# Optimization experiments

Hardware: AMD Instinct MI355X
Metric: run time of the kernel (lower is better)

The kernel has to match this reference:

```python
import jax, jax.numpy as jnp
import numpy as np
from jax import lax

N, E = 10000, 100000
IN_CH, HID, EDGE_DIM, K = 32, 64, 16, 3
DILATIONS = (1, 2, 4)


def setup_inputs() -> dict:
    key = jax.random.key(0)
    ks = jax.random.split(key, 20)
    def nrm(k, shape, fan):
        return jax.random.normal(k, shape, jnp.float32) * (1.0 / np.sqrt(fan))
    inp = {
        "x": jax.random.normal(ks[0], (N, IN_CH), jnp.float32),
        "edge_attr": jax.random.normal(ks[1], (E, EDGE_DIM), jnp.float32),
        "h_prev": jax.random.normal(ks[2], (N, K, HID), jnp.float32),
        "edge_index": jax.random.randint(ks[3], (2, E), 0, N, jnp.int32),
        # edge-conditioning MLP: edge_dim -> 32 -> in_ch*hid
        "w1": nrm(ks[4], (EDGE_DIM, 32), EDGE_DIM), "b1": jnp.zeros((32,), jnp.float32),
        "w2": nrm(ks[5], (32, IN_CH * HID), 32), "b2": jnp.zeros((IN_CH * HID,), jnp.float32),
        # NNConv root weight + bias
        "root": nrm(ks[6], (IN_CH, HID), IN_CH), "bias": jnp.zeros((HID,), jnp.float32),
        # three dilated Conv1d layers [out, in, k]
        "tcn_w1": nrm(ks[7], (HID, HID, K), HID * K), "tcn_b1": jnp.zeros((HID,), jnp.float32),
        "tcn_w2": nrm(ks[8], (HID, HID, K), HID * K), "tcn_b2": jnp.zeros((HID,), jnp.float32),
        "tcn_w3": nrm(ks[9], (HID, HID, K), HID * K), "tcn_b3": jnp.zeros((HID,), jnp.float32),
        # output projection hid*3 -> hid
        "proj_w": nrm(ks[10], (HID * len(DILATIONS), HID), HID * len(DILATIONS)),
        "proj_b": jnp.zeros((HID,), jnp.float32),
    }
    return inp


def _conv1d_last(h, w, b, dilation):
    # h: [N, C, L], w: [O, I, K]; 'same'-style padding (K-1)*d//2, return last timestep.
    pad = (K - 1) * dilation // 2
    out = lax.conv_general_dilated(
        h, w, window_strides=(1,), padding=[(pad, pad)],
        rhs_dilation=(dilation,), dimension_numbers=("NCH", "OIH", "NCH"))
    return out[:, :, -1] + b[None, :]


def reference(x, edge_attr, h_prev, edge_index,
              w1, b1, w2, b2, root, bias,
              tcn_w1, tcn_b1, tcn_w2, tcn_b2, tcn_w3, tcn_b3,
              proj_w, proj_b):
    src, dst = edge_index[0], edge_index[1]
    n = x.shape[0]

    # --- NNConv (ECC): per-edge weight via MLP, gather -> matmul -> scatter-mean ---
    h_e = jax.nn.relu(edge_attr @ w1 + b1)                   # [E, 32]
    W_e = (h_e @ w2 + b2).reshape(-1, IN_CH, HID)            # [E, in, hid]
    msg = jnp.einsum("ei,eio->eo", x[src], W_e)             # [E, hid]
    agg = jax.ops.segment_sum(msg, dst, num_segments=n)      # [N, hid]
    cnt = jax.ops.segment_sum(jnp.ones((msg.shape[0],), msg.dtype), dst, num_segments=n)
    mean = agg / jnp.maximum(cnt, 1.0)[:, None]
    h_graph = jax.nn.relu(mean + x @ root + bias)            # [N, hid]

    # --- history update ---
    h_hist = jnp.concatenate([h_prev[:, 1:], h_graph[:, None, :]], axis=1)  # [N, K, hid]

    # --- dilated TCN stack, keep only last timestep of each branch ---
    h_in = jnp.transpose(h_hist, (0, 2, 1))                  # [N, hid, K]
    outs = [
        _conv1d_last(h_in, tcn_w1, tcn_b1, DILATIONS[0]),
        _conv1d_last(h_in, tcn_w2, tcn_b2, DILATIONS[1]),
        _conv1d_last(h_in, tcn_w3, tcn_b3, DILATIONS[2]),
    ]
    h_cat = jnp.concatenate(outs, axis=1)                    # [N, hid*3]
    h_out = h_cat @ proj_w + proj_b                          # dropout = identity (eval)
    return h_out, h_hist
```

## Files before the change

kernel.cpp:

```cpp
#include <hip/hip_runtime.h>
#include <stdint.h>

#define NN 10000
#define NE 100000
#define CHUNK 20

__device__ __forceinline__ float bu2f(uint16_t u) {
    return __uint_as_float(((uint32_t)u) << 16);
}
__device__ __forceinline__ float blo(uint32_t v) { return __uint_as_float(v << 16); }
__device__ __forceinline__ float bhi(uint32_t v) { return __uint_as_float(v & 0xffff0000u); }
__device__ __forceinline__ uint16_t f2bu(float f) {
    uint32_t u = __float_as_uint(f);
    return (uint16_t)((u + 0x7fffu + ((u >> 16) & 1u)) >> 16);
}
__device__ __forceinline__ float ldf(const void* p, size_t i, int f32) {
    return f32 ? ((const float*)p)[i] : bu2f(((const uint16_t*)p)[i]);
}
struct f8 { float v[8]; };
__device__ __forceinline__ f8 ldf8(const void* p, size_t i, int f32) {
    f8 r;
    if (f32) {
        const float4* q = (const float4*)((const float*)p + i);
        float4 a = q[0], b = q[1];
        r.v[0]=a.x; r.v[1]=a.y; r.v[2]=a.z; r.v[3]=a.w;
        r.v[4]=b.x; r.v[5]=b.y; r.v[6]=b.z; r.v[7]=b.w;
    } else {
        uint4 u = *(const uint4*)((const uint16_t*)p + i);
        r.v[0]=blo(u.x); r.v[1]=bhi(u.x); r.v[2]=blo(u.y); r.v[3]=bhi(u.y);
        r.v[4]=blo(u.z); r.v[5]=bhi(u.z); r.v[6]=blo(u.w); r.v[7]=bhi(u.w);
    }
    return r;
}
__device__ __forceinline__ void stf(void* p, size_t i, float v, int f32) {
    if (f32) ((float*)p)[i] = v;
    else ((uint16_t*)p)[i] = f2bu(v);
}
__device__ __forceinline__ int clampi(int v, int lo, int hi) {
    return min(max(v, lo), hi);
}

__global__ __launch_bounds__(256) void k_init(
    const void* __restrict__ x, float4* __restrict__ zbase, int* __restrict__ flag)
{
    int bid = blockIdx.x;
    if (bid < 657) {
        int idx = bid * 256 + threadIdx.x;
        if (idx < 168088) zbase[idx] = make_float4(0.f, 0.f, 0.f, 0.f);
    } else if (threadIdx.x == 0) {
        const uint16_t* p = (const uint16_t*)x;
        int c = 0;
        for (int i = 0; i < 1024; i++) {
            float a = fabsf(bu2f(p[i]));
            if (a > 1e-3f && a < 16.0f) c++;
        }
        *flag = (c < 870) ? 1 : 0;
    }
}

__global__ __launch_bounds__(256) void k_prep(
    const void* __restrict__ x, const void* __restrict__ root,
    const void* __restrict__ tw1, const void* __restrict__ tw2,
    const void* __restrict__ tw3,
    const void* __restrict__ tb1, const void* __restrict__ tb2,
    const void* __restrict__ tb3,
    const void* __restrict__ proj_w,
    const void* __restrict__ edge_attr, const void* __restrict__ w1,
    const void* __restrict__ b1,
    const int* __restrict__ ei, const int* __restrict__ flag,
    float* __restrict__ xs_f, float* __restrict__ root_f,
    float* __restrict__ A, float* __restrict__ B, float* __restrict__ C,
    float* __restrict__ dv,
    int* __restrict__ outdeg, int* __restrict__ indeg,
    uint16_t* __restrict__ h_edge)
{
    int bid = blockIdx.x;
    int tid = threadIdx.x;
    if (bid < 157) {
        int f32 = *flag;
        int v8 = bid * 256 + tid;
        if (v8 < 40000) {
            f8 r = ldf8(x, (size_t)v8 * 8, f32);
            float4* o = (float4*)(xs_f + (size_t)v8 * 8);
            o[0] = make_float4(r.v[0], r.v[1], r.v[2], r.v[3]);
            o[1] = make_float4(r.v[4], r.v[5], r.v[6], r.v[7]);
        }
    } else if (bid == 157) {
        int f32 = *flag;
        f8 r = ldf8(root, (size_t)tid * 8, f32);
        float4* o = (float4*)(root_f + (size_t)tid * 8);
        o[0] = make_float4(r.v[0], r.v[1], r.v[2], r.v[3]);
        o[1] = make_float4(r.v[4], r.v[5], r.v[6], r.v[7]);
    } else if (bid < 670) {
        int f32 = *flag;
        int beta = bid - 158;
        int i = beta >> 3;
        int chunk = beta & 7;
        int o = tid & 63, sub = tid >> 6;
        int cc0 = chunk * 8 + sub * 2;
        float a = 0.f, b = 0.f, c = 0.f, d = 0.f;
        #pragma unroll
        for (int m = 0; m < 2; m++) {
            int cc = cc0 + m;
            float p0 = ldf(proj_w, (size_t)cc * 64 + o, f32);
            float p1 = ldf(proj_w, (size_t)(64 + cc) * 64 + o, f32);
            float p2 = ldf(proj_w, (size_t)(128 + cc) * 64 + o, f32);
            size_t base = (size_t)cc * 192 + i * 3;
            a = fmaf(ldf(tw1, base + 1, f32), p0, a);
            a = fmaf(ldf(tw2, base + 1, f32), p1, a);
            a = fmaf(ldf(tw3, base + 1, f32), p2, a);
            b = fmaf(ldf(tw2, base + 0, f32), p1, b);
            c = fmaf(ldf(tw1, base + 0, f32), p0, c);
            if (i == 0) {
                d = fmaf(ldf(tb1, cc, f32), p0, d);
                d = fmaf(ldf(tb2, cc, f32), p1, d);
                d = fmaf(ldf(tb3, cc, f32), p2, d);
            }
        }
        unsafeAtomicAdd(&A[i * 64 + o], a);
        unsafeAtomicAdd(&B[i * 64 + o], b);
        unsafeAtomicAdd(&C[i * 64 + o], c);
        if (i == 0) unsafeAtomicAdd(&dv[o], d);
    } else if (bid < 1061) {
        int e = (bid - 670) * 256 + tid;
        if (e < NE) {
            atomicAdd(&outdeg[clampi(ei[e], 0, NN - 1)], 1);
            atomicAdd(&indeg[clampi(ei[NE + e], 0, NN - 1)], 1);
        }
    } else {
        int f32 = *flag;
        __shared__ float w1s[512];
        __shared__ float b1s[32];
        __shared__ float eas[32][16];
        int e0 = (bid - 1061) * 32;
        if (tid < 64) {
            f8 r = ldf8(w1, (size_t)tid * 8, f32);
            #pragma unroll
            for (int q = 0; q < 8; q++) w1s[tid * 8 + q] = r.v[q];
        } else if (tid < 128) {
            int t = tid - 64;
            f8 r = ldf8(edge_attr, (size_t)e0 * 16 + (size_t)t * 8, f32);
            int el = t >> 1, half = (t & 1) * 8;
            #pragma unroll
            for (int q = 0; q < 8; q++) eas[el][half + q] = r.v[q];
        } else if (tid < 160) {
            b1s[tid - 128] = ldf(b1, tid - 128, f32);
        }
        __syncthreads();
        int el = tid >> 5, j = tid & 31;
        #pragma unroll
        for (int r = 0; r < 4; r++) {
            int e = el + r * 8;
            float acc = b1s[j];
            #pragma unroll
            for (int k = 0; k < 16; k++) acc = fmaf(eas[e][k], w1s[k * 32 + j], acc);
            h_edge[(size_t)(e0 + e) * 32 + j] = f2bu(fmaxf(acc, 0.0f));
        }
    }
}

__global__ __launch_bounds__(1024) void k_scan(
    const int* __restrict__ outdeg, int* __restrict__ offs, int* __restrict__ cursor)
{
    __shared__ int sums[1024];
    const int CH = 10;
    int tid = threadIdx.x;
    int base = tid * CH;
    int v[CH];
    int s = 0;
    #pragma unroll
    for (int k = 0; k < CH; k++) {
        int i = base + k;
        int c = (i < NN) ? outdeg[i] : 0;
        v[k] = s;
        s += c;
    }
    sums[tid] = s;
    __syncthreads();
    for (int d = 1; d < 1024; d <<= 1) {
        int t = (tid >= d) ? sums[tid - d] : 0;
        __syncthreads();
        if (tid >= d) sums[tid] += t;
        __syncthreads();
    }
    int prefix = (tid == 0) ? 0 : sums[tid - 1];
    #pragma unroll
    for (int k = 0; k < CH; k++) {
        int i = base + k;
        if (i <= NN) {
            int val = prefix + v[k];
            offs[i] = val;
            if (i < NN) cursor[i] = val;
        }
    }
}

__global__ __launch_bounds__(256, 4) void k_scatT(
    const int* __restrict__ ei, int* __restrict__ cursor,
    int* __restrict__ sorted_src, int* __restrict__ sorted_dst,
    int* __restrict__ sorted_eid,
    const uint16_t* __restrict__ h_edge, uint16_t* __restrict__ h_srt, int hs_mode,
    const float* __restrict__ xs_f, const void* __restrict__ w2,
    const void* __restrict__ b2, const int* __restrict__ flag,
    uint16_t* __restrict__ T, float* __restrict__ xb)
{
    int bid = blockIdx.x;
    int tid = threadIdx.x;
    if (bid < 391) {
        int e = bid * 256 + tid;
        if (e < NE) {
            int src = clampi(ei[e], 0, NN - 1);
            int dst = clampi(ei[NE + e], 0, NN - 1);
            int pos = clampi(atomicAdd(&cursor[src], 1), 0, NE - 1);
            sorted_src[pos] = src;
            sorted_dst[pos] = dst;
            if (hs_mode) {
                const uint4* hs = (const uint4*)(h_edge + (size_t)e * 32);
                uint4* hd = (uint4*)(h_srt + (size_t)pos * 32);
                hd[0] = hs[0]; hd[1] = hs[1]; hd[2] = hs[2]; hd[3] = hs[3];
            } else {
                sorted_eid[pos] = e;
            }
        }
        return;
    }
    int f32 = *flag;
    int n0 = (bid - 391) * 8;
    __shared__ float xs[8][32];
    xs[tid >> 5][tid & 31] = xs_f[(size_t)n0 * 32 + tid];
    __syncthreads();
    int c0 = tid * 8;
    int j = c0 >> 6, o0 = c0 & 63;
    float acc[8][8];
    #pragma unroll
    for (int s = 0; s < 8; s++)
        #pragma unroll
        for (int r = 0; r < 8; r++) acc[s][r] = 0.0f;
    if (f32) {
        const float* wb = (const float*)w2 + (size_t)j * 2048 + o0;
        for (int i = 0; i < 32; i++) {
            float4 a4 = *(const float4*)(wb + i * 64);
            float4 b4 = *(const float4*)(wb + i * 64 + 4);
            #pragma unroll
            for (int s = 0; s < 8; s++) {
                float xv = xs[s][i];
                acc[s][0] = fmaf(xv, a4.x, acc[s][0]); acc[s][1] = fmaf(xv, a4.y, acc[s][1]);
                acc[s][2] = fmaf(xv, a4.z, acc[s][2]); acc[s][3] = fmaf(xv, a4.w, acc[s][3]);
                acc[s][4] = fmaf(xv, b4.x, acc[s][4]); acc[s][5] = fmaf(xv, b4.y, acc[s][5]);
                acc[s][6] = fmaf(xv, b4.z, acc[s][6]); acc[s][7] = fmaf(xv, b4.w, acc[s][7]);
            }
        }
    } else {
        const uint16_t* wb = (const uint16_t*)w2 + (size_t)j * 2048 + o0;
        for (int i = 0; i < 32; i++) {
            uint4 u = *(const uint4*)(wb + i * 64);
            float w0 = blo(u.x), w1_ = bhi(u.x), w2_ = blo(u.y), w3 = bhi(u.y);
            float w4 = blo(u.z), w5 = bhi(u.z), w6 = blo(u.w), w7 = bhi(u.w);
            #pragma unroll
            for (int s = 0; s < 8; s++) {
                float xv = xs[s][i];
                acc[s][0] = fmaf(xv, w0, acc[s][0]); acc[s][1] = fmaf(xv, w1_, acc[s][1]);
                acc[s][2] = fmaf(xv, w2_, acc[s][2]); acc[s][3] = fmaf(xv, w3, acc[s][3]);
                acc[s][4] = fmaf(xv, w4, acc[s][4]); acc[s][5] = fmaf(xv, w5, acc[s][5]);
                acc[s][6] = fmaf(xv, w6, acc[s][6]); acc[s][7] = fmaf(xv, w7, acc[s][7]);
            }
        }
    }
    #pragma unroll
    for (int s = 0; s < 8; s++) {
        uint4 ov;
        ov.x = ((uint32_t)f2bu(acc[s][1]) << 16) | f2bu(acc[s][0]);
        ov.y = ((uint32_t)f2bu(acc[s][3]) << 16) | f2bu(acc[s][2]);
        ov.z = ((uint32_t)f2bu(acc[s][5]) << 16) | f2bu(acc[s][4]);
        ov.w = ((uint32_t)f2bu(acc[s][7]) << 16) | f2bu(acc[s][6]);
        *(uint4*)(T + (size_t)(n0 + s) * 2048 + c0) = ov;
    }
    int o = tid & 63;
    if (f32) {
        const float* b2f = (const float*)b2;
        #pragma unroll
        for (int h = 0; h < 2; h++) {
            int s = (tid >> 6) + h * 4;
            float a = 0.0f;
            #pragma unroll
            for (int i = 0; i < 32; i++)
                a = fmaf(xs[s][i], b2f[i * 64 + o], a);
            xb[(size_t)(n0 + s) * 64 + o] = a;
        }
    } else {
        const uint16_t* b2u = (const uint16_t*)b2;
        #pragma unroll
        for (int h = 0; h < 2; h++) {
            int s = (tid >> 6) + h * 4;
            float a = 0.0f;
            #pragma unroll
            for (int i = 0; i < 32; i++)
                a = fmaf(xs[s][i], bu2f(b2u[i * 64 + o]), a);
            xb[(size_t)(n0 + s) * 64 + o] = a;
        }
    }
}

__global__ __launch_bounds__(256) void k_msg_g(
    const uint16_t* __restrict__ h_edge, const uint16_t* __restrict__ h_srt,
    int hs_mode, const uint16_t* __restrict__ T,
    const float* __restrict__ xb, const int* __restrict__ sorted_src,
    const int* __restrict__ sorted_dst, const int* __restrict__ sorted_eid,
    float* __restrict__ agg)
{
    int wid = blockIdx.x * 4 + (threadIdx.x >> 6);
    int lane = threadIdx.x & 63;
    int p0 = wid * CHUNK;
    if (p0 >= NE) return;
    int p1 = min(p0 + CHUNK, NE);
    int cur = -1;
    float tv[32];
    float xbv = 0.0f;
    for (int p = p0; p < p1; p++) {
        int s = clampi(sorted_src[p], 0, NN - 1);
        if (s != cur) {
            cur = s;
            const uint16_t* Tr = T + (size_t)s * 2048 + lane;
            #pragma unroll
            for (int j = 0; j < 32; j++) tv[j] = bu2f(Tr[j * 64]);
            xbv = xb[(size_t)s * 64 + lane];
        }
        const uint4* hp;
        if (hs_mode) {
            hp = (const uint4*)(h_srt + (size_t)p * 32);
        } else {
            int e = clampi(sorted_eid[p], 0, NE - 1);
            hp = (const uint4*)(h_edge + (size_t)e * 32);
        }
        uint4 a = hp[0], b = hp[1], c = hp[2], d = hp[3];
        float s0 = 0.f, s1 = 0.f, s2 = 0.f, s3 = 0.f;
        s0 = fmaf(blo(a.x), tv[0],  s0); s0 = fmaf(bhi(a.x), tv[1],  s0);
        s0 = fmaf(blo(a.y), tv[2],  s0); s0 = fmaf(bhi(a.y), tv[3],  s0);
        s0 = fmaf(blo(a.z), tv[4],  s0); s0 = fmaf(bhi(a.z), tv[5],  s0);
        s0 = fmaf(blo(a.w), tv[6],  s0); s0 = fmaf(bhi(a.w), tv[7],  s0);
        s1 = fmaf(blo(b.x), tv[8],  s1); s1 = fmaf(bhi(b.x), tv[9],  s1);
        s1 = fmaf(blo(b.y), tv[10], s1); s1 = fmaf(bhi(b.y), tv[11], s1);
        s1 = fmaf(blo(b.z), tv[12], s1); s1 = fmaf(bhi(b.z), tv[13], s1);
        s1 = fmaf(blo(b.w), tv[14], s1); s1 = fmaf(bhi(b.w), tv[15], s1);
        s2 = fmaf(blo(c.x), tv[16], s2); s2 = fmaf(bhi(c.x), tv[17], s2);
        s2 = fmaf(blo(c.y), tv[18], s2); s2 = fmaf(bhi(c.y), tv[19], s2);
        s2 = fmaf(blo(c.z), tv[20], s2); s2 = fmaf(bhi(c.z), tv[21], s2);
        s2 = fmaf(blo(c.w), tv[22], s2); s2 = fmaf(bhi(c.w), tv[23], s2);
        s3 = fmaf(blo(d.x), tv[24], s3); s3 = fmaf(bhi(d.x), tv[25], s3);
        s3 = fmaf(blo(d.y), tv[26], s3); s3 = fmaf(bhi(d.y), tv[27], s3);
        s3 = fmaf(blo(d.z), tv[28], s3); s3 = fmaf(bhi(d.z), tv[29], s3);
        s3 = fmaf(blo(d.w), tv[30], s3); s3 = fmaf(bhi(d.w), tv[31], s3);
        float acc = xbv + (s0 + s1) + (s2 + s3);
        int dst = clampi(sorted_dst[p], 0, NN - 1);
        unsafeAtomicAdd(&agg[(size_t)dst * 64 + lane], acc);
    }
}

__global__ __launch_bounds__(256) void k_node_out(
    const float* __restrict__ agg, const int* __restrict__ indeg,
    const float* __restrict__ xs_f, const float* __restrict__ root_f,
    const void* __restrict__ bias, const void* __restrict__ h_prev,
    const float* __restrict__ A, const float* __restrict__ B,
    const float* __restrict__ C, const float* __restrict__ dv,
    const void* __restrict__ proj_b,
    const int* __restrict__ flag, void* __restrict__ out)
{
    int f32 = *flag;
    int tid = threadIdx.x;
    int s = tid >> 6, o = tid & 63;
    int n = blockIdx.x * 4 + s;
    const size_t O1 = (size_t)NN * 64;
    __shared__ float hg_s[4][64], hp1_s[4][64], hp2_s[4][64];

    float xr = 0.0f;
    const float* xp = xs_f + (size_t)n * 32;
    #pragma unroll
    for (int i = 0; i < 32; i++)
        xr = fmaf(xp[i], root_f[i * 64 + o], xr);
    float c = (float)indeg[n];
    float m = agg[(size_t)n * 64 + o] / fmaxf(c, 1.0f);
    float hg = fmaxf(m + xr + ldf(bias, o, f32), 0.0f);
    float hp1 = ldf(h_prev, (size_t)n * 192 + 64 + o, f32);
    float hp2 = ldf(h_prev, (size_t)n * 192 + 128 + o, f32);
    hg_s[s][o] = hg; hp1_s[s][o] = hp1; hp2_s[s][o] = hp2;
    stf(out, O1 + (size_t)n * 192 + o, hp1, f32);
    stf(out, O1 + (size_t)n * 192 + 64 + o, hp2, f32);
    stf(out, O1 + (size_t)n * 192 + 128 + o, hg, f32);
    __syncthreads();

    float accA = 0.f, accB = 0.f, accC = 0.f;
    #pragma unroll 8
    for (int i = 0; i < 64; i++) {
        accA = fmaf(hg_s[s][i],  A[i * 64 + o], accA);
        accB = fmaf(hp1_s[s][i], B[i * 64 + o], accB);
        accC = fmaf(hp2_s[s][i], C[i * 64 + o], accC);
    }
    float acc = dv[o] + ldf(proj_b, o, f32) + (accA + accB) + accC;
    stf(out, (size_t)n * 64 + o, acc, f32);
}

static inline size_t align64(size_t v) { return (v + 63) & ~(size_t)63; }

extern "C" void kernel_launch(void* const* d_in, const int* in_sizes, int n_in,
                              void* d_out, int out_size, void* d_ws, size_t ws_size,
                              hipStream_t stream) {
    const void* x         = d_in[0];
    const void* edge_attr = d_in[1];
    const void* h_prev    = d_in[2];
    const int*  ei        = (const int*)d_in[3];
    const void* w1     = d_in[4];
    const void* b1     = d_in[5];
    const void* w2     = d_in[6];
    const void* b2     = d_in[7];
    const void* root   = d_in[8];
    const void* bias   = d_in[9];
    const void* tw1    = d_in[10];
    const void* tb1    = d_in[11];
    const void* tw2    = d_in[12];
    const void* tb2    = d_in[13];
    const void* tw3    = d_in[14];
    const void* tb3    = d_in[15];
    const void* proj_w = d_in[16];
    const void* proj_b = d_in[17];

    char* ws = (char*)d_ws;
    size_t off = 0;
    uint16_t* T      = (uint16_t*)(ws + off); off = align64(off + (size_t)NN * 2048 * 2);
    uint16_t* h_edge = (uint16_t*)(ws + off); off = align64(off + (size_t)NE * 32 * 2);
    float* xs_f   = (float*)(ws + off); off = align64(off + (size_t)NN * 32 * 4);
    float* root_f = (float*)(ws + off); off = align64(off + (size_t)2048 * 4);
    float* xb     = (float*)(ws + off); off = align64(off + (size_t)NN * 64 * 4);
    size_t zero_base = off;
    float* agg    = (float*)(ws + off); off = align64(off + (size_t)NN * 64 * 4);
    int* indeg    = (int*)(ws + off);   off = align64(off + (size_t)NN * 4);
    int* outdeg   = (int*)(ws + off);   off = align64(off + (size_t)NN * 4);
    float* Amat   = (float*)(ws + off); off = align64(off + (size_t)4096 * 4);
    float* Bmat   = (float*)(ws + off); off = align64(off + (size_t)4096 * 4);
    float* Cmat   = (float*)(ws + off); off = align64(off + (size_t)4096 * 4);
    float* dvec   = (float*)(ws + off); off = align64(off + (size_t)64 * 4);
    int* offs        = (int*)(ws + off); off = align64(off + (size_t)(NN + 1) * 4);
    int* cursor      = (int*)(ws + off); off = align64(off + (size_t)NN * 4);
    int* sorted_src  = (int*)(ws + off); off = align64(off + (size_t)NE * 4);
    int* sorted_dst  = (int*)(ws + off); off = align64(off + (size_t)NE * 4);
    int* sorted_eid  = (int*)(ws + off); off = align64(off + (size_t)NE * 4);
    int* flag        = (int*)(ws + off); off = align64(off + 64);
    uint16_t* h_srt  = (uint16_t*)(ws + off);
    size_t off_end = off + (size_t)NE * 32 * 2;
    int hs_mode = (off_end <= ws_size) ? 1 : 0;

    k_init<<<658, 256, 0, stream>>>(x, (float4*)((char*)d_ws + zero_base), flag);
    k_prep<<<4186, 256, 0, stream>>>(x, root, tw1, tw2, tw3, tb1, tb2, tb3,
                                     proj_w, edge_attr, w1, b1, ei, flag,
                                     xs_f, root_f, Amat, Bmat, Cmat, dvec,
                                     outdeg, indeg, h_edge);
    k_scan<<<1, 1024, 0, stream>>>(outdeg, offs, cursor);
    k_scatT<<<391 + NN / 8, 256, 0, stream>>>(ei, cursor, sorted_src, sorted_dst,
                                              sorted_eid, h_edge, h_srt, hs_mode,
                                              xs_f, w2, b2, flag, T, xb);
    k_msg_g<<<(NE / CHUNK + 3) / 4, 256, 0, stream>>>(h_edge, h_srt, hs_mode, T, xb,
                                                      sorted_src, sorted_dst,
                                                      sorted_eid, agg);
    k_node_out<<<NN / 4, 256, 0, stream>>>(agg, indeg, xs_f, root_f, bias, h_prev,
                                           Amat, Bmat, Cmat, dvec, proj_b, flag, d_out);
}
```

Baseline: 225.9 us.

## Move per-node T/xb precompute into prep kernel and prefetch edges in message loop

Moves the per-node x·W2 (T) and x·b2 (xb) computation out of the scatter kernel into extra blocks of the prep kernel, reading x directly, so it overlaps with other prep work and the scatter kernel becomes a lightweight sort. The message kernel now software-prefetches the next edge's hidden vector and source index, and halves CHUNK to give more parallel blocks. The edge MLP caches w1 columns in registers, and the prep kernel gains a launch-bounds occupancy hint. The trade-offs are more atomic contention on agg from smaller chunks and higher register pressure in prep.

```diff
diff --git a/kernel.cpp b/kernel.cpp
--- a/kernel.cpp
+++ b/kernel.cpp
@@ -3,7 +3,7 @@
 
 #define NN 10000
 #define NE 100000
-#define CHUNK 20
+#define CHUNK 10
 
 __device__ __forceinline__ float bu2f(uint16_t u) {
     return __uint_as_float(((uint32_t)u) << 16);
@@ -58,7 +58,7 @@
     }
 }
 
-__global__ __launch_bounds__(256) void k_prep(
+__global__ __launch_bounds__(256, 4) void k_prep(
     const void* __restrict__ x, const void* __restrict__ root,
     const void* __restrict__ tw1, const void* __restrict__ tw2,
     const void* __restrict__ tw3,
@@ -67,12 +67,14 @@
     const void* __restrict__ proj_w,
     const void* __restrict__ edge_attr, const void* __restrict__ w1,
     const void* __restrict__ b1,
+    const void* __restrict__ w2, const void* __restrict__ b2,
     const int* __restrict__ ei, const int* __restrict__ flag,
     float* __restrict__ xs_f, float* __restrict__ root_f,
     float* __restrict__ A, float* __restrict__ B, float* __restrict__ C,
     float* __restrict__ dv,
     int* __restrict__ outdeg, int* __restrict__ indeg,
-    uint16_t* __restrict__ h_edge)
+    uint16_t* __restrict__ h_edge,
+    uint16_t* __restrict__ T, float* __restrict__ xb)
 {
     int bid = blockIdx.x;
     int tid = threadIdx.x;
@@ -127,7 +129,7 @@
             atomicAdd(&outdeg[clampi(ei[e], 0, NN - 1)], 1);
             atomicAdd(&indeg[clampi(ei[NE + e], 0, NN - 1)], 1);
         }
-    } else {
+    } else if (bid < 4186) {
         int f32 = *flag;
         __shared__ float w1s[512];
         __shared__ float b1s[32];
@@ -148,13 +150,98 @@
         }
         __syncthreads();
         int el = tid >> 5, j = tid & 31;
+        float wreg[16];
+        #pragma unroll
+        for (int k = 0; k < 16; k++) wreg[k] = w1s[k * 32 + j];
+        float bj = b1s[j];
         #pragma unroll
         for (int r = 0; r < 4; r++) {
             int e = el + r * 8;
-            float acc = b1s[j];
-            #pragma unroll
-            for (int k = 0; k < 16; k++) acc = fmaf(eas[e][k], w1s[k * 32 + j], acc);
+            float acc = bj;
+            #pragma unroll
+            for (int k = 0; k < 16; k++) acc = fmaf(eas[e][k], wreg[k], acc);
             h_edge[(size_t)(e0 + e) * 32 + j] = f2bu(fmaxf(acc, 0.0f));
+        }
+    } else {
+        int f32 = *flag;
+        int n0 = (bid - 4186) * 8;
+        __shared__ float xs[8][32];
+        if (tid < 32) {
+            f8 r = ldf8(x, (size_t)n0 * 32 + (size_t)tid * 8, f32);
+            int base = tid * 8;
+            #pragma unroll
+            for (int q = 0; q < 8; q++) xs[(base + q) >> 5][(base + q) & 31] = r.v[q];
+        }
+        __syncthreads();
+        int c0 = tid * 8;
+        int j = c0 >> 6, o0 = c0 & 63;
+        float acc[8][8];
+        #pragma unroll
+        for (int s = 0; s < 8; s++)
+            #pragma unroll
+            for (int r = 0; r < 8; r++) acc[s][r] = 0.0f;
+        if (f32) {
+            const float* wb = (const float*)w2 + (size_t)j * 2048 + o0;
+            for (int i = 0; i < 32; i++) {
+                float4 a4 = *(const float4*)(wb + i * 64);
+                float4 b4 = *(const float4*)(wb + i * 64 + 4);
+                #pragma unroll
+                for (int s = 0; s < 8; s++) {
+                    float xv = xs[s][i];
+                    acc[s][0] = fmaf(xv, a4.x, acc[s][0]); acc[s][1] = fmaf(xv, a4.y, acc[s][1]);
+                    acc[s][2] = fmaf(xv, a4.z, acc[s][2]); acc[s][3] = fmaf(xv, a4.w, acc[s][3]);
+                    acc[s][4] = fmaf(xv, b4.x, acc[s][4]); acc[s][5] = fmaf(xv, b4.y, acc[s][5]);
+                    acc[s][6] = fmaf(xv, b4.z, acc[s][6]); acc[s][7] = fmaf(xv, b4.w, acc[s][7]);
+                }
+            }
+        } else {
+            const uint16_t* wb = (const uint16_t*)w2 + (size_t)j * 2048 + o0;
+            for (int i = 0; i < 32; i++) {
+                uint4 u = *(const uint4*)(wb + i * 64);
+                float w0 = blo(u.x), w1_ = bhi(u.x), w2_ = blo(u.y), w3 = bhi(u.y);
+                float w4 = blo(u.z), w5 = bhi(u.z), w6 = blo(u.w), w7 = bhi(u.w);
+                #pragma unroll
+                for (int s = 0; s < 8; s++) {
+                    float xv = xs[s][i];
+                    acc[s][0] = fmaf(xv, w0, acc[s][0]); acc[s][1] = fmaf(xv, w1_, acc[s][1]);
+                    acc[s][2] = fmaf(xv, w2_, acc[s][2]); acc[s][3] = fmaf(xv, w3, acc[s][3]);
+                    acc[s][4] = fmaf(xv, w4, acc[s][4]); acc[s][5] = fmaf(xv, w5, acc[s][5]);
+                    acc[s][6] = fmaf(xv, w6, acc[s][6]); acc[s][7] = fmaf(xv, w7, acc[s][7]);
+                }
+            }
+        }
+        #pragma unroll
+        for (int s = 0; s < 8; s++) {
+            uint4 ov;
+            ov.x = ((uint32_t)f2bu(acc[s][1]) << 16) | f2bu(acc[s][0]);
+            ov.y = ((uint32_t)f2bu(acc[s][3]) << 16) | f2bu(acc[s][2]);
+            ov.z = ((uint32_t)f2bu(acc[s][5]) << 16) | f2bu(acc[s][4]);
+            ov.w = ((uint32_t)f2bu(acc[s][7]) << 16) | f2bu(acc[s][6]);
+            *(uint4*)(T + (size_t)(n0 + s) * 2048 + c0) = ov;
+        }
+        int o = tid & 63;
+        if (f32) {
+            const float* b2f = (const float*)b2;
+            #pragma unroll
+            for (int h = 0; h < 2; h++) {
+                int s = (tid >> 6) + h * 4;
+                float a = 0.0f;
+                #pragma unroll
+                for (int i = 0; i < 32; i++)
+                    a = fmaf(xs[s][i], b2f[i * 64 + o], a);
+                xb[(size_t)(n0 + s) * 64 + o] = a;
+            }
+        } else {
+            const uint16_t* b2u = (const uint16_t*)b2;
+            #pragma unroll
+            for (int h = 0; h < 2; h++) {
+                int s = (tid >> 6) + h * 4;
+                float a = 0.0f;
+                #pragma unroll
+                for (int i = 0; i < 32; i++)
+                    a = fmaf(xs[s][i], bu2f(b2u[i * 64 + o]), a);
+                xb[(size_t)(n0 + s) * 64 + o] = a;
+            }
         }
     }
 }
@@ -195,108 +282,25 @@
     }
 }
 
-__global__ __launch_bounds__(256, 4) void k_scatT(
+__global__ __launch_bounds__(256) void k_scat(
     const int* __restrict__ ei, int* __restrict__ cursor,
     int* __restrict__ sorted_src, int* __restrict__ sorted_dst,
     int* __restrict__ sorted_eid,
-    const uint16_t* __restrict__ h_edge, uint16_t* __restrict__ h_srt, int hs_mode,
-    const float* __restrict__ xs_f, const void* __restrict__ w2,
-    const void* __restrict__ b2, const int* __restrict__ flag,
-    uint16_t* __restrict__ T, float* __restrict__ xb)
-{
-    int bid = blockIdx.x;
-    int tid = threadIdx.x;
-    if (bid < 391) {
-        int e = bid * 256 + tid;
-        if (e < NE) {
-            int src = clampi(ei[e], 0, NN - 1);
-            int dst = clampi(ei[NE + e], 0, NN - 1);
-            int pos = clampi(atomicAdd(&cursor[src], 1), 0, NE - 1);
-            sorted_src[pos] = src;
-            sorted_dst[pos] = dst;
-            if (hs_mode) {
-                const uint4* hs = (const uint4*)(h_edge + (size_t)e * 32);
-                uint4* hd = (uint4*)(h_srt + (size_t)pos * 32);
-                hd[0] = hs[0]; hd[1] = hs[1]; hd[2] = hs[2]; hd[3] = hs[3];
-            } else {
-                sorted_eid[pos] = e;
-            }
-        }
-        return;
-    }
-    int f32 = *flag;
-    int n0 = (bid - 391) * 8;
-    __shared__ float xs[8][32];
-    xs[tid >> 5][tid & 31] = xs_f[(size_t)n0 * 32 + tid];
-    __syncthreads();
-    int c0 = tid * 8;
-    int j = c0 >> 6, o0 = c0 & 63;
-    float acc[8][8];
-    #pragma unroll
-    for (int s = 0; s < 8; s++)
-        #pragma unroll
-        for (int r = 0; r < 8; r++) acc[s][r] = 0.0f;
-    if (f32) {
-        const float* wb = (const float*)w2 + (size_t)j * 2048 + o0;
-        for (int i = 0; i < 32; i++) {
-            float4 a4 = *(const float4*)(wb + i * 64);
-            float4 b4 = *(const float4*)(wb + i * 64 + 4);
-            #pragma unroll
-            for (int s = 0; s < 8; s++) {
-                float xv = xs[s][i];
-                acc[s][0] = fmaf(xv, a4.x, acc[s][0]); acc[s][1] = fmaf(xv, a4.y, acc[s][1]);
-                acc[s][2] = fmaf(xv, a4.z, acc[s][2]); acc[s][3] = fmaf(xv, a4.w, acc[s][3]);
-                acc[s][4] = fmaf(xv, b4.x, acc[s][4]); acc[s][5] = fmaf(xv, b4.y, acc[s][5]);
-                acc[s][6] = fmaf(xv, b4.z, acc[s][6]); acc[s][7] = fmaf(xv, b4.w, acc[s][7]);
-            }
-        }
-    } else {
-        const uint16_t* wb = (const uint16_t*)w2 + (size_t)j * 2048 + o0;
-        for (int i = 0; i < 32; i++) {
-            uint4 u = *(const uint4*)(wb + i * 64);
-            float w0 = blo(u.x), w1_ = bhi(u.x), w2_ = blo(u.y), w3 = bhi(u.y);
-            float w4 = blo(u.z), w5 = bhi(u.z), w6 = blo(u.w), w7 = bhi(u.w);
-            #pragma unroll
-            for (int s = 0; s < 8; s++) {
-                float xv = xs[s][i];
-                acc[s][0] = fmaf(xv, w0, acc[s][0]); acc[s][1] = fmaf(xv, w1_, acc[s][1]);
-                acc[s][2] = fmaf(xv, w2_, acc[s][2]); acc[s][3] = fmaf(xv, w3, acc[s][3]);
-                acc[s][4] = fmaf(xv, w4, acc[s][4]); acc[s][5] = fmaf(xv, w5, acc[s][5]);
-                acc[s][6] = fmaf(xv, w6, acc[s][6]); acc[s][7] = fmaf(xv, w7, acc[s][7]);
-            }
-        }
-    }
-    #pragma unroll
-    for (int s = 0; s < 8; s++) {
-        uint4 ov;
-        ov.x = ((uint32_t)f2bu(acc[s][1]) << 16) | f2bu(acc[s][0]);
-        ov.y = ((uint32_t)f2bu(acc[s][3]) << 16) | f2bu(acc[s][2]);
-        ov.z = ((uint32_t)f2bu(acc[s][5]) << 16) | f2bu(acc[s][4]);
-        ov.w = ((uint32_t)f2bu(acc[s][7]) << 16) | f2bu(acc[s][6]);
-        *(uint4*)(T + (size_t)(n0 + s) * 2048 + c0) = ov;
-    }
-    int o = tid & 63;
-    if (f32) {
-        const float* b2f = (const float*)b2;
-        #pragma unroll
-        for (int h = 0; h < 2; h++) {
-            int s = (tid >> 6) + h * 4;
-            float a = 0.0f;
-            #pragma unroll
-            for (int i = 0; i < 32; i++)
-                a = fmaf(xs[s][i], b2f[i * 64 + o], a);
-            xb[(size_t)(n0 + s) * 64 + o] = a;
-        }
-    } else {
-        const uint16_t* b2u = (const uint16_t*)b2;
-        #pragma unroll
-        for (int h = 0; h < 2; h++) {
-            int s = (tid >> 6) + h * 4;
-            float a = 0.0f;
-            #pragma unroll
-            for (int i = 0; i < 32; i++)
-                a = fmaf(xs[s][i], bu2f(b2u[i * 64 + o]), a);
-            xb[(size_t)(n0 + s) * 64 + o] = a;
+    const uint16_t* __restrict__ h_edge, uint16_t* __restrict__ h_srt, int hs_mode)
+{
+    int e = blockIdx.x * 256 + threadIdx.x;
+    if (e < NE) {
+        int src = clampi(ei[e], 0, NN - 1);
+        int dst = clampi(ei[NE + e], 0, NN - 1);
+        int pos = clampi(atomicAdd(&cursor[src], 1), 0, NE - 1);
+        sorted_src[pos] = src;
+        sorted_dst[pos] = dst;
+        if (hs_mode) {
+            const uint4* hs = (const uint4*)(h_edge + (size_t)e * 32);
+            uint4* hd = (uint4*)(h_srt + (size_t)pos * 32);
+            hd[0] = hs[0]; hd[1] = hs[1]; hd[2] = hs[2]; hd[3] = hs[3];
+        } else {
+            sorted_eid[pos] = e;
         }
     }
 }
@@ -316,8 +320,22 @@
     int cur = -1;
     float tv[32];
     float xbv = 0.0f;
+    int sN = clampi(sorted_src[p0], 0, NN - 1);
+    const uint4* hq;
+    if (hs_mode) hq = (const uint4*)(h_srt + (size_t)p0 * 32);
+    else hq = (const uint4*)(h_edge + (size_t)clampi(sorted_eid[p0], 0, NE - 1) * 32);
+    uint4 na = hq[0], nb = hq[1], nc = hq[2], nd = hq[3];
     for (int p = p0; p < p1; p++) {
-        int s = clampi(sorted_src[p], 0, NN - 1);
+        int s = sN;
+        uint4 a = na, b = nb, c = nc, d = nd;
+        int dst = clampi(sorted_dst[p], 0, NN - 1);
+        if (p + 1 < p1) {
+            sN = clampi(sorted_src[p + 1], 0, NN - 1);
+            const uint4* h2;
+            if (hs_mode) h2 = (const uint4*)(h_srt + (size_t)(p + 1) * 32);
+            else h2 = (const uint4*)(h_edge + (size_t)clampi(sorted_eid[p + 1], 0, NE - 1) * 32);
+            na = h2[0]; nb = h2[1]; nc = h2[2]; nd = h2[3];
+        }
         if (s != cur) {
             cur = s;
             const uint16_t* Tr = T + (size_t)s * 2048 + lane;
@@ -325,14 +343,6 @@
             for (int j = 0; j < 32; j++) tv[j] = bu2f(Tr[j * 64]);
             xbv = xb[(size_t)s * 64 + lane];
         }
-        const uint4* hp;
-        if (hs_mode) {
-            hp = (const uint4*)(h_srt + (size_t)p * 32);
-        } else {
-            int e = clampi(sorted_eid[p], 0, NE - 1);
-            hp = (const uint4*)(h_edge + (size_t)e * 32);
-        }
-        uint4 a = hp[0], b = hp[1], c = hp[2], d = hp[3];
         float s0 = 0.f, s1 = 0.f, s2 = 0.f, s3 = 0.f;
         s0 = fmaf(blo(a.x), tv[0],  s0); s0 = fmaf(bhi(a.x), tv[1],  s0);
         s0 = fmaf(blo(a.y), tv[2],  s0); s0 = fmaf(bhi(a.y), tv[3],  s0);
@@ -351,7 +361,6 @@
         s3 = fmaf(blo(d.z), tv[28], s3); s3 = fmaf(bhi(d.z), tv[29], s3);
         s3 = fmaf(blo(d.w), tv[30], s3); s3 = fmaf(bhi(d.w), tv[31], s3);
         float acc = xbv + (s0 + s1) + (s2 + s3);
-        int dst = clampi(sorted_dst[p], 0, NN - 1);
         unsafeAtomicAdd(&agg[(size_t)dst * 64 + lane], acc);
     }
 }
@@ -449,14 +458,13 @@
     int hs_mode = (off_end <= ws_size) ? 1 : 0;
 
     k_init<<<658, 256, 0, stream>>>(x, (float4*)((char*)d_ws + zero_base), flag);
-    k_prep<<<4186, 256, 0, stream>>>(x, root, tw1, tw2, tw3, tb1, tb2, tb3,
-                                     proj_w, edge_attr, w1, b1, ei, flag,
+    k_prep<<<5436, 256, 0, stream>>>(x, root, tw1, tw2, tw3, tb1, tb2, tb3,
+                                     proj_w, edge_attr, w1, b1, w2, b2, ei, flag,
                                      xs_f, root_f, Amat, Bmat, Cmat, dvec,
-                                     outdeg, indeg, h_edge);
+                                     outdeg, indeg, h_edge, T, xb);
     k_scan<<<1, 1024, 0, stream>>>(outdeg, offs, cursor);
-    k_scatT<<<391 + NN / 8, 256, 0, stream>>>(ei, cursor, sorted_src, sorted_dst,
-                                              sorted_eid, h_edge, h_srt, hs_mode,
-                                              xs_f, w2, b2, flag, T, xb);
+    k_scat<<<391, 256, 0, stream>>>(ei, cursor, sorted_src, sorted_dst,
+                                    sorted_eid, h_edge, h_srt, hs_mode);
     k_msg_g<<<(NE / CHUNK + 3) / 4, 256, 0, stream>>>(h_edge, h_srt, hs_mode, T, xb,
                                                       sorted_src, sorted_dst,
                                                       sorted_eid, agg);
```

Result: slower. 232.7 us (+3.0%).
